# Kernel tuning notes

Measured on AMD Instinct MI355X. Metric: run time of the kernel, lower is better.

Reference implementation:

```python
import jax, jax.numpy as jnp
import numpy as np

SOFTMAX_SCALE = 10.0  # self.softmax_scale
EPS = 1e-4


def _patches(img, k=3):
    # img: [H, W, C] -> patches laid out as conv filters [k, k, C, L], L = H*W
    # (matches tf.image.extract_patches SAME/stride1 + reshape + transpose([0,2,3,4,1]))
    H, W, C = img.shape
    pad = (k - 1) // 2
    xp = jnp.pad(img, ((pad, pad), (pad, pad), (0, 0)))
    pat = jnp.stack([jnp.stack([xp[p:p + H, q:q + W] for q in range(k)]) for p in range(k)])
    # pat: [k, k, H, W, C] -> [k, k, C, H*W]; L index is row-major (h*W + w) like TF reshape
    return pat.transpose(0, 1, 4, 2, 3).reshape(k, k, C, H * W)


def _normed(p):
    # per-patch L2 normalization over the k*k*C axes (axes 0,1,2)
    return p / jnp.maximum(jnp.sqrt(jnp.sum(p * p, axis=(0, 1, 2))), EPS)


def _corr_recon(a, b, k=3):
    # a, b: [H', W', C] shifted feature maps
    Hp, Wp, C = a.shape
    L = Hp * Wp
    pa = _patches(a, k)  # [k,k,C,L]
    pb = _patches(b, k)
    y = (_normed(pa) * _normed(pb)).reshape(k * k * C, L)
    att = y.T @ y                                   # [L, L] patch-correlation scores
    att = jax.nn.softmax(att.reshape(1, Hp, Wp, L) * SOFTMAX_SCALE, axis=3)
    dn = ('NHWC', 'HWIO', 'NHWC')
    # tf.nn.conv2d_transpose(att, filters=[k,k,C,L], stride=1, SAME); rate=1 so /rate**2 is a no-op
    ya = jax.lax.conv_transpose(att, pa, (1, 1), 'SAME', dimension_numbers=dn, transpose_kernel=True)[0]
    yb = jax.lax.conv_transpose(att, pb, (1, 1), 'SAME', dimension_numbers=dn, transpose_kernel=True)[0]
    return ya, yb  # each [H', W', C]


def _ecattn_single(xi):
    # xi: [H, W, C]
    left, right = xi[:-1], xi[1:]          # vertical neighbor pair, [H-1, W, C]
    top, bottom = xi[:, 1:], xi[:, :-1]    # horizontal neighbor pair, [H, W-1, C]
    yl, yr = _corr_recon(left, right)
    ylr = jnp.concatenate([yr[:1], (yr[1:] + yl[:-1]) * 0.5, yl[-1:]], axis=0)   # [H, W, C]
    yt, yb = _corr_recon(top, bottom)
    ytb = jnp.concatenate([yt[:, :1], (yt[:, 1:] + yb[:, :-1]) * 0.5, yb[:, -1:]], axis=1)  # [H, W, C]
    return (ylr + ytb) * 0.5


def setup_inputs() -> dict:
    key = jax.random.key(0)
    k1, k2 = jax.random.split(key)
    B, H, W, C = 4, 32, 32, 256
    x = jax.random.normal(k1, (B, H, W, C), dtype=jnp.float32)
    mask = jax.random.uniform(k2, (B, H, W, 1), dtype=jnp.float32)
    return {'x': x, 'mask': mask}


def reference(x, mask):
    # mask is accepted by the layer's call() but unused inside contextualAttention
    return jax.vmap(_ecattn_single)(x)
```

## Files before the change

kernel.cpp:

```cpp
#include <hip/hip_runtime.h>


typedef _Float16 half8 __attribute__((ext_vector_type(8)));
typedef _Float16 half8u __attribute__((ext_vector_type(8), aligned(4)));
typedef _Float16 half4h __attribute__((ext_vector_type(4)));
typedef _Float16 half4u __attribute__((ext_vector_type(4), aligned(8)));
typedef float floatx4 __attribute__((ext_vector_type(4)));

constexpr int NL = 992, NC = 256, NC2 = 512;
constexpr int NLL = NL * NL;
constexpr int OFF_ABT = 0;
constexpr int OFF_MH  = OFF_ABT + NL * NC2 / 2;
constexpr int OFF_SA  = OFF_MH + NL * NC / 2;
constexpr int OFF_SB  = OFF_SA + 1024;
constexpr int OFF_INV = OFF_SA + 2048;
constexpr int OFF_Y   = OFF_SA + 3072;
constexpr int OFF_B0  = OFF_Y + NL * NC2;
constexpr int OFF_B1  = OFF_B0 + NLL / 2;
constexpr int TSTRIDE = OFF_B1 + NLL / 2;

__device__ __forceinline__ void gload16(const void* g, void* l) {
    __builtin_amdgcn_global_load_lds(
        (const __attribute__((address_space(1))) unsigned int*)g,
        (__attribute__((address_space(3))) unsigned int*)(unsigned long)(uintptr_t)l,
        16, 0, 0);
}

__global__ __launch_bounds__(256) void k_prep(const float* __restrict__ x,
                                              float* __restrict__ ws) {
    const int t = blockIdx.x & 7;
    const int l = blockIdx.x >> 3;
    const int s = t >> 1, o = t & 1;
    int aoff, boff;
    if (o == 0) {
        const int lh = l >> 5, lw = l & 31;
        aoff = ((s * 32 + lh) * 32 + lw) * NC;
        boff = ((s * 32 + lh + 1) * 32 + lw) * NC;
    } else {
        const int lh = l / 31, lw = l - lh * 31;
        aoff = ((s * 32 + lh) * 32 + lw + 1) * NC;
        boff = ((s * 32 + lh) * 32 + lw) * NC;
    }
    float* wst = ws + (size_t)t * TSTRIDE;
    const int c = threadIdx.x;
    const float av = x[aoff + c];
    const float bv = x[boff + c];
    ((_Float16*)(wst + OFF_MH))[l * NC + c] = (_Float16)(av * bv);
    float ra = av * av, rb = bv * bv;
#pragma unroll
    for (int off = 32; off > 0; off >>= 1) {
        ra += __shfl_down(ra, off);
        rb += __shfl_down(rb, off);
    }
    __shared__ float shA[4], shB[4];
    const int wave = threadIdx.x >> 6, lane = threadIdx.x & 63;
    if (lane == 0) { shA[wave] = ra; shB[wave] = rb; }
    __syncthreads();
    if (threadIdx.x == 0) {
        wst[OFF_SA + l] = shA[0] + shA[1] + shA[2] + shA[3];
        wst[OFF_SB + l] = shB[0] + shB[1] + shB[2] + shB[3];
    }
}

__global__ __launch_bounds__(256) void k_abt(const float* __restrict__ x,
                                             float* __restrict__ ws) {
    const int t = blockIdx.x & 7;
    const int u = blockIdx.x >> 3;
    const int cbk = u / 31;
    const int c0 = cbk * 32;
    const int l0 = (u - cbk * 31) * 32;
    const int s = t >> 1, o = t & 1;
    float* wst = ws + (size_t)t * TSTRIDE;
    _Float16* __restrict__ ABt = (_Float16*)(wst + OFF_ABT);
    __shared__ float T[32 * 33];
    const int tid = threadIdx.x;
    const bool isB = (c0 >= 256);
    const int cb = isB ? c0 - 256 : c0;
    {
        const int li = tid >> 3, cq = tid & 7;
        const int l = l0 + li;
        int xoff;
        if (o == 0) {
            const int lh = l >> 5, lw = l & 31;
            xoff = isB ? ((s * 32 + lh + 1) * 32 + lw) : ((s * 32 + lh) * 32 + lw);
        } else {
            const int lh = l / 31, lw = l - lh * 31;
            xoff = isB ? ((s * 32 + lh) * 32 + lw) : ((s * 32 + lh) * 32 + lw + 1);
        }
        const float4 v = *(const float4*)&x[xoff * NC + cb + cq * 4];
        T[(cq * 4 + 0) * 33 + li] = v.x;
        T[(cq * 4 + 1) * 33 + li] = v.y;
        T[(cq * 4 + 2) * 33 + li] = v.z;
        T[(cq * 4 + 3) * 33 + li] = v.w;
    }
    __syncthreads();
    {
        const int ci = tid >> 3, lq = tid & 7;
        half4h h;
        h.x = (_Float16)T[ci * 33 + lq * 4 + 0];
        h.y = (_Float16)T[ci * 33 + lq * 4 + 1];
        h.z = (_Float16)T[ci * 33 + lq * 4 + 2];
        h.w = (_Float16)T[ci * 33 + lq * 4 + 3];
        *(half4h*)&ABt[(c0 + ci) * NL + l0 + lq * 4] = h;
    }
}

__global__ __launch_bounds__(1024) void k_inv(float* __restrict__ ws) {
    const int t = blockIdx.x;
    const int l = threadIdx.x;
    if (l >= NL) return;
    const int o = t & 1;
    const int Hp = o ? 32 : 31, Wp = o ? 31 : 32;
    float* wst = ws + (size_t)t * TSTRIDE;
    const int h = l / Wp, w = l - h * Wp;
    float na2 = 0.0f, nb2 = 0.0f;
#pragma unroll
    for (int dh = -1; dh <= 1; ++dh)
#pragma unroll
        for (int dw = -1; dw <= 1; ++dw) {
            const int hh = h + dh, ww = w + dw;
            if ((unsigned)hh < (unsigned)Hp && (unsigned)ww < (unsigned)Wp) {
                const int ll = hh * Wp + ww;
                na2 += wst[OFF_SA + ll];
                nb2 += wst[OFF_SB + ll];
            }
        }
    const float na = fmaxf(sqrtf(na2), 1e-4f);
    const float nb = fmaxf(sqrtf(nb2), 1e-4f);
    wst[OFF_INV + l] = 1.0f / (na * nb);
}

__global__ __launch_bounds__(256) void k_gram(float* __restrict__ ws) {
    const int t = blockIdx.x & 7;
    const int u = blockIdx.x >> 3;
    const int i0 = (u >> 3) * 128, j0 = (u & 7) * 128;
    float* wst = ws + (size_t)t * TSTRIDE;
    const _Float16* __restrict__ M = (const _Float16*)(wst + OFF_MH);
    _Float16* __restrict__ S = (_Float16*)(wst + OFF_B0);
    __shared__ __align__(16) _Float16 As[128 * 32];
    __shared__ __align__(16) _Float16 Bs[128 * 32];
    const int tid = threadIdx.x;
    const int wave = tid >> 6, lane = tid & 63;
    const int wm = wave & 1, wn = wave >> 1;
    const int l15 = lane & 15, quad = lane >> 4;
    floatx4 acc[4][4] = {};
    const int srow = tid >> 2;
    const int scol = (tid & 3) * 8;
    for (int k0 = 0; k0 < NC; k0 += 32) {
        __syncthreads();
        if (i0 + srow < NL)      gload16(&M[(i0 + srow) * NC + k0 + scol], &As[srow * 32 + scol]);
        if (i0 + 64 + srow < NL) gload16(&M[(i0 + 64 + srow) * NC + k0 + scol], &As[(64 + srow) * 32 + scol]);
        if (j0 + srow < NL)      gload16(&M[(j0 + srow) * NC + k0 + scol], &Bs[srow * 32 + scol]);
        if (j0 + 64 + srow < NL) gload16(&M[(j0 + 64 + srow) * NC + k0 + scol], &Bs[(64 + srow) * 32 + scol]);
        __syncthreads();
        half8 a[4], b[4];
#pragma unroll
        for (int mt = 0; mt < 4; ++mt) a[mt] = *(const half8*)&As[(wm * 64 + mt * 16 + l15) * 32 + quad * 8];
#pragma unroll
        for (int nt = 0; nt < 4; ++nt) b[nt] = *(const half8*)&Bs[(wn * 64 + nt * 16 + l15) * 32 + quad * 8];
#pragma unroll
        for (int mt = 0; mt < 4; ++mt)
#pragma unroll
            for (int nt = 0; nt < 4; ++nt)
                acc[mt][nt] = __builtin_amdgcn_mfma_f32_16x16x32_f16(a[mt], b[nt], acc[mt][nt], 0, 0, 0);
    }
#pragma unroll
    for (int mt = 0; mt < 4; ++mt)
#pragma unroll
        for (int nt = 0; nt < 4; ++nt)
#pragma unroll
            for (int r = 0; r < 4; ++r) {
                const int row = i0 + wm * 64 + mt * 16 + quad * 4 + r;
                const int col = j0 + wn * 64 + nt * 16 + l15;
                if (row < NL && col < NL) S[row * NL + col] = (_Float16)acc[mt][nt][r];
            }
}

template<int WP>
__device__ __forceinline__ void bandw_body(const _Float16* __restrict__ S,
                                           _Float16* __restrict__ D,
                                           const int r, const int tid) {
    if (tid >= 248) return;
    const int c0 = tid * 4;
    const int w1 = r % WP;
    const bool okm = (w1 > 0), okp = (w1 + 1 < WP);
    float acc[4];
    const half4u v0 = *(const half4u*)(S + r * NL + c0);
#pragma unroll
    for (int j = 0; j < 4; ++j) acc[j] = (float)v0[j];
    if (okm) {
        const half8u vm = *(const half8u*)(S + (r - 1) * NL + c0 - 2);
#pragma unroll
        for (int j = 0; j < 4; ++j)
            if ((c0 + j) % WP > 0) acc[j] += (float)vm[j + 1];
    }
    if (okp) {
        const half8u vp = *(const half8u*)(S + (r + 1) * NL + c0);
#pragma unroll
        for (int j = 0; j < 4; ++j)
            if ((c0 + j) % WP + 1 < WP) acc[j] += (float)vp[j + 1];
    }
    half4h o;
#pragma unroll
    for (int j = 0; j < 4; ++j) o[j] = (_Float16)acc[j];
    *(half4u*)(D + r * NL + c0) = o;
}

__global__ __launch_bounds__(256) void k_bandw(float* __restrict__ ws) {
    const int t = blockIdx.x & 7;
    const int r = blockIdx.x >> 3;
    float* wst = ws + (size_t)t * TSTRIDE;
    const _Float16* S = (const _Float16*)(wst + OFF_B0);
    _Float16* D = (_Float16*)(wst + OFF_B1);
    if (t & 1) bandw_body<31>(S, D, r, threadIdx.x);
    else       bandw_body<32>(S, D, r, threadIdx.x);
}

template<int WP, int HP>
__device__ __forceinline__ void softmax_body(float* __restrict__ wst,
                                             const int l1, const int tid) {
    const _Float16* __restrict__ Sw = (const _Float16*)(wst + OFF_B1);
    const float* __restrict__ inv = wst + OFF_INV;
    _Float16* __restrict__ Ph = (_Float16*)(wst + OFF_B0);
    constexpr int SH = WP * (NL + 1);
    constexpr int PAR = SH & 1;
    const int h1 = l1 / WP;
    const bool okm = (h1 > 0), okp = (h1 + 1 < HP);
    const float inv1 = inv[l1] * 10.0f;
    const int c0 = tid * 4;
    float lg[4] = {-3.0e38f, -3.0e38f, -3.0e38f, -3.0e38f};
    float mx = -3.0e38f;
    if (tid < 248) {
        float g[4];
        const half4u v0 = *(const half4u*)(Sw + l1 * NL + c0);
#pragma unroll
        for (int j = 0; j < 4; ++j) g[j] = (float)v0[j];
        if (okm) {
            const half8u vm = *(const half8u*)(Sw + l1 * NL + c0 - SH - PAR);
#pragma unroll
            for (int j = 0; j < 4; ++j)
                if (c0 + j >= WP) g[j] += (float)vm[j + PAR];
        }
        if (okp) {
            const half8u vp = *(const half8u*)(Sw + l1 * NL + c0 + SH - PAR);
#pragma unroll
            for (int j = 0; j < 4; ++j)
                if (c0 + j < NL - WP) g[j] += (float)vp[j + PAR];
        }
#pragma unroll
        for (int j = 0; j < 4; ++j) {
            lg[j] = g[j] * inv1 * inv[c0 + j];
            mx = fmaxf(mx, lg[j]);
        }
    }
    __shared__ float red[4];
    const int wave = tid >> 6, lane = tid & 63;
#pragma unroll
    for (int off = 32; off > 0; off >>= 1) mx = fmaxf(mx, __shfl_down(mx, off));
    if (lane == 0) red[wave] = mx;
    __syncthreads();
    mx = fmaxf(fmaxf(red[0], red[1]), fmaxf(red[2], red[3]));
    __syncthreads();
    float e[4];
    float sum = 0.0f;
#pragma unroll
    for (int j = 0; j < 4; ++j) { e[j] = __expf(lg[j] - mx); sum += e[j]; }
    if (tid >= 248) sum = 0.0f;
#pragma unroll
    for (int off = 32; off > 0; off >>= 1) sum += __shfl_down(sum, off);
    if (lane == 0) red[wave] = sum;
    __syncthreads();
    sum = red[0] + red[1] + red[2] + red[3];
    const float rs = 1.0f / sum;
    if (tid < 248) {
        half4h o;
#pragma unroll
        for (int j = 0; j < 4; ++j) o[j] = (_Float16)(e[j] * rs);
        *(half4u*)(Ph + l1 * NL + c0) = o;
    }
}

__global__ __launch_bounds__(256) void k_softmax(float* __restrict__ ws) {
    const int t = blockIdx.x & 7;
    const int l1 = blockIdx.x >> 3;
    float* wst = ws + (size_t)t * TSTRIDE;
    if (t & 1) softmax_body<31, 32>(wst, l1, threadIdx.x);
    else       softmax_body<32, 31>(wst, l1, threadIdx.x);
}

template<int WP, int HP>
__device__ __forceinline__ void band9p_body(float* __restrict__ wst,
                                            const int m, const int tid) {
    if (tid >= 248) return;
    const _Float16* __restrict__ P = (const _Float16*)(wst + OFF_B0);
    _Float16* __restrict__ W = (_Float16*)(wst + OFF_B1);
    const int c0 = tid * 4;
    const int hm = m / WP, wm = m % WP;
    int hc[4], wc[4];
#pragma unroll
    for (int j = 0; j < 4; ++j) { hc[j] = (c0 + j) / WP; wc[j] = (c0 + j) % WP; }
    float acc[4] = {0.f, 0.f, 0.f, 0.f};
    const _Float16* base = P + m * NL + c0;
#pragma unroll
    for (int dh = -1; dh <= 1; ++dh) {
        const bool oh1 = (unsigned)(hm + dh) < (unsigned)HP;
#pragma unroll
        for (int dw = -1; dw <= 1; ++dw) {
            const int sh = dh * WP + dw;
            const int par = sh & 1;
            const bool ok1 = oh1 && (unsigned)(wm + dw) < (unsigned)WP;
            const half8u v = *(const half8u*)(base + sh * (NL + 1) - par);
#pragma unroll
            for (int j = 0; j < 4; ++j) {
                const bool ok = ok1 && (unsigned)(hc[j] + dh) < (unsigned)HP &&
                                       (unsigned)(wc[j] + dw) < (unsigned)WP;
                if (ok) acc[j] += (float)v[j + par];
            }
        }
    }
    half4h o;
#pragma unroll
    for (int j = 0; j < 4; ++j) o[j] = (_Float16)acc[j];
    *(half4u*)(W + m * NL + c0) = o;
}

__global__ __launch_bounds__(256) void k_band9p(float* __restrict__ ws) {
    const int t = blockIdx.x & 7;
    const int m = blockIdx.x >> 3;
    float* wst = ws + (size_t)t * TSTRIDE;
    if (t & 1) band9p_body<31, 32>(wst, m, threadIdx.x);
    else       band9p_body<32, 31>(wst, m, threadIdx.x);
}

__global__ __launch_bounds__(256) void k_recon(float* __restrict__ ws) {
    const int t = blockIdx.x & 7;
    const int u = blockIdx.x >> 3;
    const int i0 = (u >> 2) * 128, j0 = (u & 3) * 128;
    float* wst = ws + (size_t)t * TSTRIDE;
    const _Float16* __restrict__ Wm = (const _Float16*)(wst + OFF_B1);
    const _Float16* __restrict__ ABt = (const _Float16*)(wst + OFF_ABT);
    float* __restrict__ Y = wst + OFF_Y;
    __shared__ __align__(16) _Float16 As[128 * 32];
    __shared__ __align__(16) _Float16 Bs[128 * 32];
    const int tid = threadIdx.x;
    const int wave = tid >> 6, lane = tid & 63;
    const int wm = wave & 1, wn = wave >> 1;
    const int l15 = lane & 15, quad = lane >> 4;
    floatx4 acc[4][4] = {};
    const int srow = tid >> 2;
    const int scol = (tid & 3) * 8;
    for (int k0 = 0; k0 < NL; k0 += 32) {
        __syncthreads();
        if (i0 + srow < NL)      gload16(&Wm[(i0 + srow) * NL + k0 + scol], &As[srow * 32 + scol]);
        if (i0 + 64 + srow < NL) gload16(&Wm[(i0 + 64 + srow) * NL + k0 + scol], &As[(64 + srow) * 32 + scol]);
        gload16(&ABt[(j0 + srow) * NL + k0 + scol], &Bs[srow * 32 + scol]);
        gload16(&ABt[(j0 + 64 + srow) * NL + k0 + scol], &Bs[(64 + srow) * 32 + scol]);
        __syncthreads();
        half8 a[4], b[4];
#pragma unroll
        for (int mt = 0; mt < 4; ++mt) a[mt] = *(const half8*)&As[(wm * 64 + mt * 16 + l15) * 32 + quad * 8];
#pragma unroll
        for (int nt = 0; nt < 4; ++nt) b[nt] = *(const half8*)&Bs[(wn * 64 + nt * 16 + l15) * 32 + quad * 8];
#pragma unroll
        for (int mt = 0; mt < 4; ++mt)
#pragma unroll
            for (int nt = 0; nt < 4; ++nt)
                acc[mt][nt] = __builtin_amdgcn_mfma_f32_16x16x32_f16(a[mt], b[nt], acc[mt][nt], 0, 0, 0);
    }
#pragma unroll
    for (int mt = 0; mt < 4; ++mt)
#pragma unroll
        for (int nt = 0; nt < 4; ++nt)
#pragma unroll
            for (int r = 0; r < 4; ++r) {
                const int row = i0 + wm * 64 + mt * 16 + quad * 4 + r;
                const int col = j0 + wn * 64 + nt * 16 + l15;
                if (row < NL) Y[row * NC2 + col] = acc[mt][nt][r];
            }
}

__global__ __launch_bounds__(256) void k_combine(float* __restrict__ out,
                                                 const float* __restrict__ ws) {
    const int idx = blockIdx.x;
    const int s = idx >> 10;
    const int hw = idx & 1023;
    const int h = hw >> 5, w = hw & 31;
    const int c = threadIdx.x;
    const float* Ylr = ws + (size_t)(2 * s) * TSTRIDE + OFF_Y;
    const float* Ytb = ws + (size_t)(2 * s + 1) * TSTRIDE + OFF_Y;
    float v = 0.0f;
    if (h < 31) v += Ylr[(h * 32 + w) * NC2 + NC + c] * (h == 0 ? 1.0f : 0.5f);
    if (h >= 1) v += Ylr[((h - 1) * 32 + w) * NC2 + c] * (h == 31 ? 1.0f : 0.5f);
    if (w < 31) v += Ytb[(h * 31 + w) * NC2 + c] * (w == 0 ? 1.0f : 0.5f);
    if (w >= 1) v += Ytb[(h * 31 + (w - 1)) * NC2 + NC + c] * (w == 31 ? 1.0f : 0.5f);
    out[(size_t)idx * NC + c] = v * 0.5f;
}

extern "C" void kernel_launch(void* const* d_in, const int* in_sizes, int n_in,
                              void* d_out, int out_size, void* d_ws, size_t ws_size,
                              hipStream_t stream) {
    const float* x = (const float*)d_in[0];
    float* out = (float*)d_out;
    float* ws = (float*)d_ws;

    hipLaunchKernelGGL(k_prep,    dim3(8 * NL),  dim3(256),  0, stream, x, ws);
    hipLaunchKernelGGL(k_abt,     dim3(8 * 496), dim3(256),  0, stream, x, ws);
    hipLaunchKernelGGL(k_inv,     dim3(8),       dim3(1024), 0, stream, ws);
    hipLaunchKernelGGL(k_gram,    dim3(8 * 64),  dim3(256),  0, stream, ws);
    hipLaunchKernelGGL(k_bandw,   dim3(8 * NL),  dim3(256),  0, stream, ws);
    hipLaunchKernelGGL(k_softmax, dim3(8 * NL),  dim3(256),  0, stream, ws);
    hipLaunchKernelGGL(k_band9p,  dim3(8 * NL),  dim3(256),  0, stream, ws);
    hipLaunchKernelGGL(k_recon,   dim3(8 * 32),  dim3(256),  0, stream, ws);
    hipLaunchKernelGGL(k_combine, dim3(4096),    dim3(256),  0, stream, out, ws);
}
```

Measured before the change: 154.8 us.

## Fuse prep with transpose staging and fold band-sum into softmax

Merges k_prep and k_abt into one k_stage kernel. It reads each x row once and produces the fp16 elementwise product, the squared norms and the transposed A/B matrices together. It also removes the separate k_bandw pass: softmax now gathers all 9 diagonal-shifted entries of the Gram matrix directly instead of reading a pre-banded intermediate, and the buffer roles of B0 and B1 are swapped to match. This drops two launches and a full NL×NL fp16 write/read round trip. The cost is 9 unaligned loads per element in softmax and a kernel with only 248 blocks and serialized syncthreads across 8 channel chunks.

```diff
diff --git a/kernel.cpp b/kernel.cpp
--- a/kernel.cpp
+++ b/kernel.cpp
@@ -26,82 +26,63 @@
         16, 0, 0);
 }
 
-__global__ __launch_bounds__(256) void k_prep(const float* __restrict__ x,
-                                              float* __restrict__ ws) {
-    const int t = blockIdx.x & 7;
-    const int l = blockIdx.x >> 3;
+__global__ __launch_bounds__(256) void k_stage(const float* __restrict__ x,
+                                               float* __restrict__ ws) {
+    const int t = blockIdx.x & 7;
+    const int l0 = (blockIdx.x >> 3) * 32;
     const int s = t >> 1, o = t & 1;
+    float* wst = ws + (size_t)t * TSTRIDE;
+    _Float16* __restrict__ ABt = (_Float16*)(wst + OFF_ABT);
+    _Float16* __restrict__ Mh = (_Float16*)(wst + OFF_MH);
+    __shared__ float Ta[32 * 33], Tb[32 * 33];
+    const int tid = threadIdx.x;
+    const int li = tid >> 3, cq = tid & 7;
+    const int l = l0 + li;
     int aoff, boff;
     if (o == 0) {
         const int lh = l >> 5, lw = l & 31;
         aoff = ((s * 32 + lh) * 32 + lw) * NC;
-        boff = ((s * 32 + lh + 1) * 32 + lw) * NC;
+        boff = aoff + 32 * NC;
     } else {
         const int lh = l / 31, lw = l - lh * 31;
-        aoff = ((s * 32 + lh) * 32 + lw + 1) * NC;
         boff = ((s * 32 + lh) * 32 + lw) * NC;
-    }
-    float* wst = ws + (size_t)t * TSTRIDE;
-    const int c = threadIdx.x;
-    const float av = x[aoff + c];
-    const float bv = x[boff + c];
-    ((_Float16*)(wst + OFF_MH))[l * NC + c] = (_Float16)(av * bv);
-    float ra = av * av, rb = bv * bv;
-#pragma unroll
-    for (int off = 32; off > 0; off >>= 1) {
-        ra += __shfl_down(ra, off);
-        rb += __shfl_down(rb, off);
-    }
-    __shared__ float shA[4], shB[4];
-    const int wave = threadIdx.x >> 6, lane = threadIdx.x & 63;
-    if (lane == 0) { shA[wave] = ra; shB[wave] = rb; }
-    __syncthreads();
-    if (threadIdx.x == 0) {
-        wst[OFF_SA + l] = shA[0] + shA[1] + shA[2] + shA[3];
-        wst[OFF_SB + l] = shB[0] + shB[1] + shB[2] + shB[3];
-    }
-}
-
-__global__ __launch_bounds__(256) void k_abt(const float* __restrict__ x,
-                                             float* __restrict__ ws) {
-    const int t = blockIdx.x & 7;
-    const int u = blockIdx.x >> 3;
-    const int cbk = u / 31;
-    const int c0 = cbk * 32;
-    const int l0 = (u - cbk * 31) * 32;
-    const int s = t >> 1, o = t & 1;
-    float* wst = ws + (size_t)t * TSTRIDE;
-    _Float16* __restrict__ ABt = (_Float16*)(wst + OFF_ABT);
-    __shared__ float T[32 * 33];
-    const int tid = threadIdx.x;
-    const bool isB = (c0 >= 256);
-    const int cb = isB ? c0 - 256 : c0;
-    {
-        const int li = tid >> 3, cq = tid & 7;
-        const int l = l0 + li;
-        int xoff;
-        if (o == 0) {
-            const int lh = l >> 5, lw = l & 31;
-            xoff = isB ? ((s * 32 + lh + 1) * 32 + lw) : ((s * 32 + lh) * 32 + lw);
-        } else {
-            const int lh = l / 31, lw = l - lh * 31;
-            xoff = isB ? ((s * 32 + lh) * 32 + lw) : ((s * 32 + lh) * 32 + lw + 1);
-        }
-        const float4 v = *(const float4*)&x[xoff * NC + cb + cq * 4];
-        T[(cq * 4 + 0) * 33 + li] = v.x;
-        T[(cq * 4 + 1) * 33 + li] = v.y;
-        T[(cq * 4 + 2) * 33 + li] = v.z;
-        T[(cq * 4 + 3) * 33 + li] = v.w;
-    }
-    __syncthreads();
-    {
-        const int ci = tid >> 3, lq = tid & 7;
-        half4h h;
-        h.x = (_Float16)T[ci * 33 + lq * 4 + 0];
-        h.y = (_Float16)T[ci * 33 + lq * 4 + 1];
-        h.z = (_Float16)T[ci * 33 + lq * 4 + 2];
-        h.w = (_Float16)T[ci * 33 + lq * 4 + 3];
-        *(half4h*)&ABt[(c0 + ci) * NL + l0 + lq * 4] = h;
+        aoff = boff + NC;
+    }
+    float sa = 0.0f, sb = 0.0f;
+    for (int cc = 0; cc < 8; ++cc) {
+        const int c0 = cc * 32;
+        const float4 a4 = *(const float4*)&x[aoff + c0 + cq * 4];
+        const float4 b4 = *(const float4*)&x[boff + c0 + cq * 4];
+        half4h m;
+        m[0] = (_Float16)(a4.x * b4.x); m[1] = (_Float16)(a4.y * b4.y);
+        m[2] = (_Float16)(a4.z * b4.z); m[3] = (_Float16)(a4.w * b4.w);
+        *(half4u*)&Mh[l * NC + c0 + cq * 4] = m;
+        sa += a4.x * a4.x + a4.y * a4.y + a4.z * a4.z + a4.w * a4.w;
+        sb += b4.x * b4.x + b4.y * b4.y + b4.z * b4.z + b4.w * b4.w;
+        __syncthreads();
+        Ta[(cq * 4 + 0) * 33 + li] = a4.x; Tb[(cq * 4 + 0) * 33 + li] = b4.x;
+        Ta[(cq * 4 + 1) * 33 + li] = a4.y; Tb[(cq * 4 + 1) * 33 + li] = b4.y;
+        Ta[(cq * 4 + 2) * 33 + li] = a4.z; Tb[(cq * 4 + 2) * 33 + li] = b4.z;
+        Ta[(cq * 4 + 3) * 33 + li] = a4.w; Tb[(cq * 4 + 3) * 33 + li] = b4.w;
+        __syncthreads();
+        const int ci = li, lq = cq;
+        half4h ha, hb;
+#pragma unroll
+        for (int j = 0; j < 4; ++j) {
+            ha[j] = (_Float16)Ta[ci * 33 + lq * 4 + j];
+            hb[j] = (_Float16)Tb[ci * 33 + lq * 4 + j];
+        }
+        *(half4u*)&ABt[(c0 + ci) * NL + l0 + lq * 4] = ha;
+        *(half4u*)&ABt[(NC + c0 + ci) * NL + l0 + lq * 4] = hb;
+    }
+#pragma unroll
+    for (int off = 4; off > 0; off >>= 1) {
+        sa += __shfl_down(sa, off, 8);
+        sb += __shfl_down(sb, off, 8);
+    }
+    if (cq == 0) {
+        wst[OFF_SA + l] = sa;
+        wst[OFF_SB + l] = sb;
     }
 }
 
@@ -176,77 +157,40 @@
             }
 }
 
-template<int WP>
-__device__ __forceinline__ void bandw_body(const _Float16* __restrict__ S,
-                                           _Float16* __restrict__ D,
-                                           const int r, const int tid) {
-    if (tid >= 248) return;
+template<int WP, int HP>
+__device__ __forceinline__ void softmax9_body(float* __restrict__ wst,
+                                              const int l1, const int tid) {
+    const _Float16* __restrict__ S = (const _Float16*)(wst + OFF_B0);
+    const float* __restrict__ inv = wst + OFF_INV;
+    _Float16* __restrict__ Ph = (_Float16*)(wst + OFF_B1);
     const int c0 = tid * 4;
-    const int w1 = r % WP;
-    const bool okm = (w1 > 0), okp = (w1 + 1 < WP);
-    float acc[4];
-    const half4u v0 = *(const half4u*)(S + r * NL + c0);
-#pragma unroll
-    for (int j = 0; j < 4; ++j) acc[j] = (float)v0[j];
-    if (okm) {
-        const half8u vm = *(const half8u*)(S + (r - 1) * NL + c0 - 2);
-#pragma unroll
-        for (int j = 0; j < 4; ++j)
-            if ((c0 + j) % WP > 0) acc[j] += (float)vm[j + 1];
-    }
-    if (okp) {
-        const half8u vp = *(const half8u*)(S + (r + 1) * NL + c0);
-#pragma unroll
-        for (int j = 0; j < 4; ++j)
-            if ((c0 + j) % WP + 1 < WP) acc[j] += (float)vp[j + 1];
-    }
-    half4h o;
-#pragma unroll
-    for (int j = 0; j < 4; ++j) o[j] = (_Float16)acc[j];
-    *(half4u*)(D + r * NL + c0) = o;
-}
-
-__global__ __launch_bounds__(256) void k_bandw(float* __restrict__ ws) {
-    const int t = blockIdx.x & 7;
-    const int r = blockIdx.x >> 3;
-    float* wst = ws + (size_t)t * TSTRIDE;
-    const _Float16* S = (const _Float16*)(wst + OFF_B0);
-    _Float16* D = (_Float16*)(wst + OFF_B1);
-    if (t & 1) bandw_body<31>(S, D, r, threadIdx.x);
-    else       bandw_body<32>(S, D, r, threadIdx.x);
-}
-
-template<int WP, int HP>
-__device__ __forceinline__ void softmax_body(float* __restrict__ wst,
-                                             const int l1, const int tid) {
-    const _Float16* __restrict__ Sw = (const _Float16*)(wst + OFF_B1);
-    const float* __restrict__ inv = wst + OFF_INV;
-    _Float16* __restrict__ Ph = (_Float16*)(wst + OFF_B0);
-    constexpr int SH = WP * (NL + 1);
-    constexpr int PAR = SH & 1;
-    const int h1 = l1 / WP;
-    const bool okm = (h1 > 0), okp = (h1 + 1 < HP);
-    const float inv1 = inv[l1] * 10.0f;
-    const int c0 = tid * 4;
+    const int h1 = l1 / WP, w1 = l1 % WP;
     float lg[4] = {-3.0e38f, -3.0e38f, -3.0e38f, -3.0e38f};
     float mx = -3.0e38f;
     if (tid < 248) {
-        float g[4];
-        const half4u v0 = *(const half4u*)(Sw + l1 * NL + c0);
-#pragma unroll
-        for (int j = 0; j < 4; ++j) g[j] = (float)v0[j];
-        if (okm) {
-            const half8u vm = *(const half8u*)(Sw + l1 * NL + c0 - SH - PAR);
-#pragma unroll
-            for (int j = 0; j < 4; ++j)
-                if (c0 + j >= WP) g[j] += (float)vm[j + PAR];
-        }
-        if (okp) {
-            const half8u vp = *(const half8u*)(Sw + l1 * NL + c0 + SH - PAR);
-#pragma unroll
-            for (int j = 0; j < 4; ++j)
-                if (c0 + j < NL - WP) g[j] += (float)vp[j + PAR];
-        }
+        int hc[4], wc[4];
+#pragma unroll
+        for (int j = 0; j < 4; ++j) { hc[j] = (c0 + j) / WP; wc[j] = (c0 + j) % WP; }
+        float g[4] = {0.f, 0.f, 0.f, 0.f};
+        const _Float16* base = S + l1 * NL + c0;
+#pragma unroll
+        for (int dh = -1; dh <= 1; ++dh) {
+            const bool oh1 = (unsigned)(h1 + dh) < (unsigned)HP;
+#pragma unroll
+            for (int dw = -1; dw <= 1; ++dw) {
+                const int sh = dh * WP + dw;
+                const int par = sh & 1;
+                const bool ok1 = oh1 && (unsigned)(w1 + dw) < (unsigned)WP;
+                const half8u v = *(const half8u*)(base + sh * (NL + 1) - par);
+#pragma unroll
+                for (int j = 0; j < 4; ++j) {
+                    const bool ok = ok1 && (unsigned)(hc[j] + dh) < (unsigned)HP &&
+                                           (unsigned)(wc[j] + dw) < (unsigned)WP;
+                    if (ok) g[j] += (float)v[j + par];
+                }
+            }
+        }
+        const float inv1 = inv[l1] * 10.0f;
 #pragma unroll
         for (int j = 0; j < 4; ++j) {
             lg[j] = g[j] * inv1 * inv[c0 + j];
@@ -280,20 +224,20 @@
     }
 }
 
-__global__ __launch_bounds__(256) void k_softmax(float* __restrict__ ws) {
+__global__ __launch_bounds__(256) void k_softmax9(float* __restrict__ ws) {
     const int t = blockIdx.x & 7;
     const int l1 = blockIdx.x >> 3;
     float* wst = ws + (size_t)t * TSTRIDE;
-    if (t & 1) softmax_body<31, 32>(wst, l1, threadIdx.x);
-    else       softmax_body<32, 31>(wst, l1, threadIdx.x);
+    if (t & 1) softmax9_body<31, 32>(wst, l1, threadIdx.x);
+    else       softmax9_body<32, 31>(wst, l1, threadIdx.x);
 }
 
 template<int WP, int HP>
 __device__ __forceinline__ void band9p_body(float* __restrict__ wst,
                                             const int m, const int tid) {
     if (tid >= 248) return;
-    const _Float16* __restrict__ P = (const _Float16*)(wst + OFF_B0);
-    _Float16* __restrict__ W = (_Float16*)(wst + OFF_B1);
+    const _Float16* __restrict__ P = (const _Float16*)(wst + OFF_B1);
+    _Float16* __restrict__ W = (_Float16*)(wst + OFF_B0);
     const int c0 = tid * 4;
     const int hm = m / WP, wm = m % WP;
     int hc[4], wc[4];
@@ -337,7 +281,7 @@
     const int u = blockIdx.x >> 3;
     const int i0 = (u >> 2) * 128, j0 = (u & 3) * 128;
     float* wst = ws + (size_t)t * TSTRIDE;
-    const _Float16* __restrict__ Wm = (const _Float16*)(wst + OFF_B1);
+    const _Float16* __restrict__ Wm = (const _Float16*)(wst + OFF_B0);
     const _Float16* __restrict__ ABt = (const _Float16*)(wst + OFF_ABT);
     float* __restrict__ Y = wst + OFF_Y;
     __shared__ __align__(16) _Float16 As[128 * 32];
@@ -403,13 +347,11 @@
     float* out = (float*)d_out;
     float* ws = (float*)d_ws;
 
-    hipLaunchKernelGGL(k_prep,    dim3(8 * NL),  dim3(256),  0, stream, x, ws);
-    hipLaunchKernelGGL(k_abt,     dim3(8 * 496), dim3(256),  0, stream, x, ws);
-    hipLaunchKernelGGL(k_inv,     dim3(8),       dim3(1024), 0, stream, ws);
-    hipLaunchKernelGGL(k_gram,    dim3(8 * 64),  dim3(256),  0, stream, ws);
-    hipLaunchKernelGGL(k_bandw,   dim3(8 * NL),  dim3(256),  0, stream, ws);
-    hipLaunchKernelGGL(k_softmax, dim3(8 * NL),  dim3(256),  0, stream, ws);
-    hipLaunchKernelGGL(k_band9p,  dim3(8 * NL),  dim3(256),  0, stream, ws);
-    hipLaunchKernelGGL(k_recon,   dim3(8 * 32),  dim3(256),  0, stream, ws);
-    hipLaunchKernelGGL(k_combine, dim3(4096),    dim3(256),  0, stream, out, ws);
-}
+    hipLaunchKernelGGL(k_stage,    dim3(8 * 31), dim3(256),  0, stream, x, ws);
+    hipLaunchKernelGGL(k_inv,      dim3(8),      dim3(1024), 0, stream, ws);
+    hipLaunchKernelGGL(k_gram,     dim3(8 * 64), dim3(256),  0, stream, ws);
+    hipLaunchKernelGGL(k_softmax9, dim3(8 * NL), dim3(256),  0, stream, ws);
+    hipLaunchKernelGGL(k_band9p,   dim3(8 * NL), dim3(256),  0, stream, ws);
+    hipLaunchKernelGGL(k_recon,    dim3(8 * 32), dim3(256),  0, stream, ws);
+    hipLaunchKernelGGL(k_combine,  dim3(4096),   dim3(256),  0, stream, out, ws);
+}
```

Result: faster. 149.4 us (-3.5%).
